# Kernel optimization log

Measured on AMD Instinct MI355X. Metric: run time of the kernel, lower is better.

The kernel has to match this reference:

```python
import jax, jax.numpy as jnp
import numpy as np

H = 50  # hidden size (hardcoded in the torch module)

def lstm_cell(h, c, xt, Wih, Whh, bih, bhh):
    # xt: [B, D]; gates packed PyTorch-style: i, f, g, o each of size H
    gates = xt @ Wih.T + h @ Whh.T + bih + bhh  # [B, 4H]
    i, f, g, o = jnp.split(gates, 4, axis=-1)
    i = jax.nn.sigmoid(i)
    f = jax.nn.sigmoid(f)
    g = jnp.tanh(g)
    o = jax.nn.sigmoid(o)
    c_new = f * c + i * g
    h_new = o * jnp.tanh(c_new)
    return h_new, c_new

def lstm_last_hidden(x, Wih, Whh, bih, bhh):
    # x: [B, T, D] -> final hidden state h_T: [B, H] (zero init state)
    B = x.shape[0]
    h0 = jnp.zeros((B, H), dtype=x.dtype)
    c0 = jnp.zeros((B, H), dtype=x.dtype)
    def step(carry, xt):
        h, c = carry
        h, c = lstm_cell(h, c, xt, Wih, Whh, bih, bhh)
        return (h, c), None
    (hT, _), _ = jax.lax.scan(step, (h0, c0), jnp.swapaxes(x, 0, 1))
    return hT

def setup_inputs() -> dict:
    key = jax.random.key(0)
    ks = jax.random.split(key, 11)
    s = 1.0 / np.sqrt(H)  # PyTorch LSTM/Linear init scale
    u = lambda k, shape: jax.random.uniform(k, shape, jnp.float32, -s, s)
    return {
        'x': jax.random.normal(ks[0], (2048, 1024, 1), jnp.float32),
        'lstm1_Wih': u(ks[1], (4 * H, 1)),
        'lstm1_Whh': u(ks[2], (4 * H, H)),
        'lstm1_bih': u(ks[3], (4 * H,)),
        'lstm1_bhh': u(ks[4], (4 * H,)),
        'lstm2_Wih': u(ks[5], (4 * H, H)),
        'lstm2_Whh': u(ks[6], (4 * H, H)),
        'lstm2_bih': u(ks[7], (4 * H,)),
        'lstm2_bhh': u(ks[8], (4 * H,)),
        'fc_W': u(ks[9], (1, H)),
        'fc_b': u(ks[10], (1,)),
    }

def reference(x, lstm1_Wih, lstm1_Whh, lstm1_bih, lstm1_bhh,
              lstm2_Wih, lstm2_Whh, lstm2_bih, lstm2_bhh, fc_W, fc_b):
    # lstm1 over full sequence; only the last timestep output is used downstream
    h1 = lstm_last_hidden(x, lstm1_Wih, lstm1_Whh, lstm1_bih, lstm1_bhh)  # [B, H]
    # lstm2 sees a length-1 sequence starting from zero state -> one cell step
    B = x.shape[0]
    z = jnp.zeros((B, H), dtype=x.dtype)
    h2, _ = lstm_cell(z, z, h1, lstm2_Wih, lstm2_Whh, lstm2_bih, lstm2_bhh)  # [B, H]
    return h2 @ fc_W.T + fc_b  # [B, 1]
```

## Files before the change

### kernel.cpp

```cpp
#include <hip/hip_runtime.h>

#define HH 50
#define TT 1024
#define BT 4
#define NB (2048 / BT)
#define XSTF 1028
#define HST 72

typedef _Float16 half8 __attribute__((ext_vector_type(8)));
typedef float f32x4 __attribute__((ext_vector_type(4)));

union H8 { half8 v; _Float16 h[8]; unsigned short u[8]; unsigned int i[4]; };

__device__ __forceinline__ float rcp_f(float x) { return __builtin_amdgcn_rcpf(x); }

#if __has_builtin(__builtin_amdgcn_exp2f)
__device__ __forceinline__ float exp2_f(float x) { return __builtin_amdgcn_exp2f(x); }
#else
__device__ __forceinline__ float exp2_f(float x) { return __expf(0.6931471805599453f * x); }
#endif

#define L2E   1.4426950408889634f
#define L2E2  2.8853900817779268f

__device__ __forceinline__ float sigm_n(float a) {
    return rcp_f(1.0f + exp2_f(a));
}
__device__ __forceinline__ float tanh_p(float a) {
    return __builtin_fmaf(-2.0f, rcp_f(1.0f + exp2_f(a)), 1.0f);
}
__device__ __forceinline__ unsigned short f2h(float f) {
    return __builtin_bit_cast(unsigned short, (_Float16)f);
}

__global__ __launch_bounds__(256) void lstm_mfma_kernel(
    const float* __restrict__ x,
    const float* __restrict__ wih1, const float* __restrict__ whh1,
    const float* __restrict__ bih1, const float* __restrict__ bhh1,
    const float* __restrict__ wih2,
    const float* __restrict__ bih2, const float* __restrict__ bhh2,
    const float* __restrict__ fcw,  const float* __restrict__ fcb,
    float* __restrict__ out)
{
    __shared__ float xs[BT * XSTF];
    __shared__ __align__(16) unsigned short hb[2][16 * HST];
    __shared__ float h2s[BT * 52];

    const int tid  = threadIdx.x;
    const int wv   = tid >> 6;
    const int js   = wv;
    const int lane = tid & 63;
    const int l16  = lane & 15;
    const int quad = lane >> 4;
    const int j    = js * 16 + l16;
    const bool jv  = (j < HH);
    const bool q2  = (quad == 2);
    const int b0   = blockIdx.x * BT;

    H8 bw[4][2];
    #pragma unroll
    for (int t4 = 0; t4 < 4; ++t4) {
        const float sc = (t4 == 2) ? L2E2 : -L2E;
        const int row = t4 * HH + j;
        #pragma unroll
        for (int kk = 0; kk < 2; ++kk)
            #pragma unroll
            for (int e = 0; e < 8; ++e) {
                const int k = kk * 32 + quad * 8 + e;
                const float v = (jv && k < HH) ? whh1[row * HH + k] * sc : 0.0f;
                bw[t4][kk].h[e] = (_Float16)v;
            }
        if (q2) {
            const float bsc = jv ? (bih1[row] + bhh1[row]) * sc : 0.0f;
            const _Float16 bhi = (_Float16)bsc;
            bw[t4][1].h[2] = (_Float16)(jv ? wih1[row] * sc : 0.0f);
            bw[t4][1].h[3] = bhi;
            bw[t4][1].h[4] = (_Float16)(bsc - (float)bhi);
        }
    }

    for (int i = tid; i < 2 * 16 * HST; i += 256) {
        const int col = i % HST;
        ((unsigned short*)hb)[i] = (col == 51 || col == 52) ? 0x3c00 : 0;
    }

    for (int i = tid; i < BT * (TT / 4); i += 256) {
        const int r = i >> 8, c4 = i & 255;
        const float4 q = ((const float4*)x)[((b0 + r) * TT) / 4 + c4];
        *(float4*)&xs[r * XSTF + c4 * 4] = q;
    }
    if (tid < BT * 4) xs[(tid >> 2) * XSTF + 1024 + (tid & 3)] = 0.0f;
    __syncthreads();

    const bool xw = (wv == 0) && (lane < BT);
    if (xw) hb[0][lane * HST + 50] = f2h(xs[lane * XSTF]);
    __syncthreads();

    float c = 0.f;
    const f32x4 kZ = {0.f, 0.f, 0.f, 0.f};

    auto cell = [&](float ai, float af, float ag, float ao, float& cc) -> unsigned short {
        const float Ei = exp2_f(ai), Ef = exp2_f(af), Eg = exp2_f(ag), Eo = exp2_f(ao);
        const float pf  = 1.0f + Ef;
        const float P   = (1.0f + Ei) * (1.0f + Eg);
        const float den = pf * P;
        const float num = __builtin_fmaf(cc, P, (Eg - 1.0f) * pf);
        cc = num * rcp_f(den);
        const float ac = fminf(cc * L2E2, 80.0f);
        const float Ec = exp2_f(ac);
        const float h  = (Ec - 1.0f) * rcp_f((1.0f + Eo) * (1.0f + Ec));
        return f2h(h);
    };

#define REDIST(G, PG)                                                          \
    {                                                                          \
        float xx0 = acc[G][0], xx1 = acc[G][1];                                \
        float yy0 = acc[G][2], yy1 = acc[G][3];                                \
        asm("v_permlane16_swap_b32 %0, %1" : "+v"(xx0), "+v"(xx1));            \
        asm("v_permlane16_swap_b32 %0, %1" : "+v"(yy0), "+v"(yy1));            \
        asm("v_permlane32_swap_b32 %0, %1" : "+v"(xx0), "+v"(yy0));            \
        PG = xx0;                                                              \
    }

#define STEP(T, CUR, NXT)                                                      \
    {                                                                          \
        H8 a0, a1;                                                             \
        a0.v = *(const half8*)&(CUR)[l16 * HST + quad * 8];                    \
        a1.v = *(const half8*)&(CUR)[l16 * HST + 32 + quad * 8];               \
        float xnext = 0.0f;                                                    \
        if (xw) xnext = xs[lane * XSTF + (T) + 1];                             \
        f32x4 acc[4];                                                          \
        _Pragma("unroll")                                                      \
        for (int t4 = 0; t4 < 4; ++t4) {                                       \
            acc[t4] = __builtin_amdgcn_mfma_f32_16x16x32_f16(a0.v, bw[t4][0].v, kZ, 0, 0, 0);       \
            acc[t4] = __builtin_amdgcn_mfma_f32_16x16x32_f16(a1.v, bw[t4][1].v, acc[t4], 0, 0, 0);  \
        }                                                                      \
        float p0, p1, p2, p3;                                                  \
        REDIST(0, p0) REDIST(1, p1) REDIST(2, p2) REDIST(3, p3)                \
        const unsigned short hv = cell(p0, p1, p2, p3, c);                     \
        if (jv) (NXT)[quad * HST + j] = hv;   \
        if (xw) (NXT)[lane * HST + 50] = f2h(xnext);                           \
        __syncthreads();                                                       \
    }

    for (int t = 0; t < TT; t += 2) {
        STEP(t,     hb[0], hb[1]);
        STEP(t + 1, hb[1], hb[0]);
    }
#undef STEP
#undef REDIST
    unsigned short* cur = hb[0];

    {
        H8 bw2[4][2];
        float b2[4];
        #pragma unroll
        for (int t4 = 0; t4 < 4; ++t4) {
            const float sc = (t4 == 2) ? L2E2 : -L2E;
            const int row = t4 * HH + j;
            #pragma unroll
            for (int kk = 0; kk < 2; ++kk)
                #pragma unroll
                for (int e = 0; e < 8; ++e) {
                    const int k = kk * 32 + quad * 8 + e;
                    const float v = (jv && k < HH) ? wih2[row * HH + k] * sc : 0.0f;
                    bw2[t4][kk].h[e] = (_Float16)v;
                }
            b2[t4] = jv ? (bih2[row] + bhh2[row]) * sc : 0.0f;
        }
        H8 a0, a1;
        a0.v = *(const half8*)&cur[l16 * HST + quad * 8];
        a1.v = *(const half8*)&cur[l16 * HST + 32 + quad * 8];
        f32x4 acc2[4];
        #pragma unroll
        for (int t4 = 0; t4 < 4; ++t4) {
            const f32x4 cb = {b2[t4], b2[t4], b2[t4], b2[t4]};
            acc2[t4] = __builtin_amdgcn_mfma_f32_16x16x32_f16(a0.v, bw2[t4][0].v, cb, 0, 0, 0);
            acc2[t4] = __builtin_amdgcn_mfma_f32_16x16x32_f16(a1.v, bw2[t4][1].v, acc2[t4], 0, 0, 0);
        }
        #pragma unroll
        for (int r = 0; r < 4; ++r) {
            const int b = quad * 4 + r;
            const float ig = sigm_n(acc2[0][r]);
            const float gg = tanh_p(acc2[2][r]);
            const float og = sigm_n(acc2[3][r]);
            const float cc = ig * gg;
            const float h2 = og * tanh_p(cc * L2E2);
            if (b < BT && jv) h2s[b * 52 + j] = h2;
        }
    }
    __syncthreads();

    if (tid < BT * 16) {
        const int b = tid >> 4, l = tid & 15;
        float p = 0.f;
        for (int jj = l; jj < HH; jj += 16)
            p = __builtin_fmaf(h2s[b * 52 + jj], fcw[jj], p);
        #pragma unroll
        for (int off = 8; off > 0; off >>= 1) p += __shfl_xor(p, off, 16);
        if (l == 0) out[b0 + b] = p + fcb[0];
    }
}

extern "C" void kernel_launch(void* const* d_in, const int* in_sizes, int n_in,
                              void* d_out, int out_size, void* d_ws, size_t ws_size,
                              hipStream_t stream) {
    lstm_mfma_kernel<<<NB, 256, 0, stream>>>(
        (const float*)d_in[0],
        (const float*)d_in[1], (const float*)d_in[2],
        (const float*)d_in[3], (const float*)d_in[4],
        (const float*)d_in[5],
        (const float*)d_in[7], (const float*)d_in[8],
        (const float*)d_in[9], (const float*)d_in[10],
        (float*)d_out);
}
```

Baseline: 520.4 us.

## Process eight batch rows per block with two LSTM cells per lane

Doubles the batch rows handled per block from 4 to 8, halving the grid. Each lane now computes two cell updates per step using rows of the 16-row MFMA output that were previously padding. The redistribution uses only permlane32 swaps and stores two hidden values per lane. This uses more of each MFMA and each barrier per step, at the cost of more transcendental work per lane on the serial recurrence and half as many blocks to fill the GPU.

```diff
diff --git a/kernel.cpp b/kernel.cpp
--- a/kernel.cpp
+++ b/kernel.cpp
@@ -2,7 +2,7 @@
 
 #define HH 50
 #define TT 1024
-#define BT 4
+#define BT 8
 #define NB (2048 / BT)
 #define XSTF 1028
 #define HST 72
@@ -56,6 +56,7 @@
     const bool jv  = (j < HH);
     const bool q2  = (quad == 2);
     const int b0   = blockIdx.x * BT;
+    const int  bm0   = ((quad & 1) << 2) + ((quad >> 1) << 1);
 
     H8 bw[4][2];
     #pragma unroll
@@ -96,7 +97,7 @@
     if (xw) hb[0][lane * HST + 50] = f2h(xs[lane * XSTF]);
     __syncthreads();
 
-    float c = 0.f;
+    float c0 = 0.f, c1 = 0.f;
     const f32x4 kZ = {0.f, 0.f, 0.f, 0.f};
 
     auto cell = [&](float ai, float af, float ag, float ao, float& cc) -> unsigned short {
@@ -112,14 +113,14 @@
         return f2h(h);
     };
 
-#define REDIST(G, PG)                                                          \
+#define REDIST(G, P0, P1)                                                      \
     {                                                                          \
-        float xx0 = acc[G][0], xx1 = acc[G][1];                                \
-        float yy0 = acc[G][2], yy1 = acc[G][3];                                \
-        asm("v_permlane16_swap_b32 %0, %1" : "+v"(xx0), "+v"(xx1));            \
-        asm("v_permlane16_swap_b32 %0, %1" : "+v"(yy0), "+v"(yy1));            \
-        asm("v_permlane32_swap_b32 %0, %1" : "+v"(xx0), "+v"(yy0));            \
-        PG = xx0;                                                              \
+        float a_ = acc[G][0], b_ = acc[G][1];                                  \
+        float c_ = acc[G][2], d_ = acc[G][3];                                  \
+        asm("v_permlane32_swap_b32 %0, %1" : "+v"(a_), "+v"(c_));              \
+        asm("v_permlane32_swap_b32 %0, %1" : "+v"(b_), "+v"(d_));              \
+        P0 = a_;                                                               \
+        P1 = b_;                                                               \
     }
 
 #define STEP(T, CUR, NXT)                                                      \
@@ -135,10 +136,15 @@
             acc[t4] = __builtin_amdgcn_mfma_f32_16x16x32_f16(a0.v, bw[t4][0].v, kZ, 0, 0, 0);       \
             acc[t4] = __builtin_amdgcn_mfma_f32_16x16x32_f16(a1.v, bw[t4][1].v, acc[t4], 0, 0, 0);  \
         }                                                                      \
-        float p0, p1, p2, p3;                                                  \
-        REDIST(0, p0) REDIST(1, p1) REDIST(2, p2) REDIST(3, p3)                \
-        const unsigned short hv = cell(p0, p1, p2, p3, c);                     \
-        if (jv) (NXT)[quad * HST + j] = hv;   \
+        float pi0, pi1, pf0, pf1, pg0, pg1, po0, po1;                          \
+        REDIST(0, pi0, pi1) REDIST(1, pf0, pf1)                                \
+        REDIST(2, pg0, pg1) REDIST(3, po0, po1)                                \
+        const unsigned short h0 = cell(pi0, pf0, pg0, po0, c0);                \
+        const unsigned short h1 = cell(pi1, pf1, pg1, po1, c1);                \
+        if (jv) {        \
+            (NXT)[bm0 * HST + j]       = h0;                                   \
+            (NXT)[(bm0 + 1) * HST + j] = h1;                                   \
+        }                                                                      \
         if (xw) (NXT)[lane * HST + 50] = f2h(xnext);                           \
         __syncthreads();                                                       \
     }
```

Result: faster. 432.3 us (-16.9%).
